# Kernel tuning notes

Hardware: AMD Instinct MI355X
Metric: run time of the kernel (lower is better)

## Reference

```python
import jax, jax.numpy as jnp
import numpy as np

N_NODES = 100000


def gcn_conv(x, W, b, src, dst, n_nodes):
    """PyG-style GCNConv: h = D^{-1/2} (A + I) D^{-1/2} (x @ W) + b.

    src/dst already include self-loops. Symmetric normalization with
    degrees computed on the destination index (in-degree incl. self-loop).
    """
    h = x @ W  # [N, out] - transform before propagate (cheap gather dim)
    deg = jax.ops.segment_sum(jnp.ones_like(dst, dtype=h.dtype), dst,
                              num_segments=n_nodes)  # [N]
    dinv = jnp.where(deg > 0, jax.lax.rsqrt(deg), 0.0)  # deg^{-1/2}, 0 for isolated
    norm = dinv[src] * dinv[dst]  # [E]
    msg = h[src] * norm[:, None]  # gather + normalize, [E, out]
    out = jax.ops.segment_sum(msg, dst, num_segments=n_nodes)  # scatter-sum
    return out + b


def setup_inputs() -> dict:
    key = jax.random.key(0)
    k1, k2, k3, k4 = jax.random.split(key, 4)
    in_dim, hidden, n_edges = 128, 32, 3200000
    x = jax.random.normal(k1, (N_NODES, in_dim), dtype=jnp.float32)
    edge_index = jax.random.randint(k2, (2, n_edges), 0, N_NODES, dtype=jnp.int64)
    W1 = jax.random.normal(k3, (in_dim, hidden), dtype=jnp.float32) / np.sqrt(in_dim)
    b1 = jnp.zeros((hidden,), dtype=jnp.float32)
    W2 = jax.random.normal(k4, (hidden, 1), dtype=jnp.float32) / np.sqrt(hidden)
    b2 = jnp.zeros((1,), dtype=jnp.float32)
    return {"x": x, "edge_index": edge_index, "W1": W1, "b1": b1,
            "W2": W2, "b2": b2}


def reference(x, edge_index, W1, b1, W2, b2):
    n = x.shape[0]
    loops = jnp.arange(n, dtype=edge_index.dtype)
    src = jnp.concatenate([edge_index[0], loops])  # add self-loops
    dst = jnp.concatenate([edge_index[1], loops])
    h = jax.nn.relu(gcn_conv(x, W1, b1, src, dst, n))
    out = jax.nn.sigmoid(gcn_conv(h, W2, b2, src, dst, n))
    return out.squeeze(-1)  # [N]
```

## Files before the change

kernel.cpp:

```cpp
#include <hip/hip_runtime.h>
#include <hip/hip_bf16.h>
#include <stdint.h>

#define IN_DIM 128
#define HID 32
#define CSHIFT 7
#define CNODES 128
#define CAP 4608
#define NPART 8
#define SUBCAP 672
#define TILE 4096
#define NBC_MAX 800

__device__ __forceinline__ float bf_lo(uint u) {
    uint t = u << 16; return *(float*)&t;
}
__device__ __forceinline__ float bf_hi(uint u) {
    uint t = u & 0xFFFF0000u; return *(float*)&t;
}

__global__ __launch_bounds__(256) void binB_kernel(const int* __restrict__ src,
                                                   const int* __restrict__ dst,
                                                   int* __restrict__ pcursor,
                                                   int* __restrict__ pbuf,
                                                   int e, int nbc) {
    __shared__ int pk[TILE];
    __shared__ short binsArr[TILE];
    __shared__ int hist[NBC_MAX];
    __shared__ int gbase[NBC_MAX];
    int part = blockIdx.x & (NPART - 1);
    int base = blockIdx.x * TILE;
    int cnt = min(TILE, e - base);
    if (cnt <= 0) return;
    for (int i = threadIdx.x; i < nbc; i += 256) hist[i] = 0;
    __syncthreads();
    for (int i = threadIdx.x; i < cnt; i += 256) {
        int s = __builtin_nontemporal_load(src + base + i);
        int d = __builtin_nontemporal_load(dst + base + i);
        int bin = d >> CSHIFT;
        pk[i] = s | ((d & (CNODES - 1)) << 17);
        binsArr[i] = (short)bin;
        atomicAdd(&hist[bin], 1);
    }
    __syncthreads();
    for (int i = threadIdx.x; i < nbc; i += 256) {
        int c = hist[i];
        gbase[i] = (c > 0) ? atomicAdd(&pcursor[part * nbc + i], c) : 0;
        hist[i] = 0;
    }
    __syncthreads();
    for (int i = threadIdx.x; i < cnt; i += 256) {
        int bin = binsArr[i];
        int slot = atomicAdd(&hist[bin], 1);
        int pos = gbase[bin] + slot;
        if (pos < SUBCAP)
            pbuf[(size_t)(part * nbc + bin) * SUBCAP + pos] = pk[i];
    }
}

__global__ __launch_bounds__(256) void sortmm_kernel(const int* __restrict__ pcursor,
                                                     const int* __restrict__ pbuf,
                                                     int* __restrict__ csr,
                                                     int* __restrict__ row_beg,
                                                     int* __restrict__ row_end,
                                                     float* __restrict__ dinv_g,
                                                     const float* __restrict__ x,
                                                     const float* __restrict__ W1,
                                                     __hip_bfloat16* __restrict__ h1s,
                                                     int n, int nbc) {
    int b = blockIdx.x;
    __shared__ int sbe[CAP];
    __shared__ int hist[CNODES];
    __shared__ int offs[CNODES];
    __shared__ int cur[CNODES];
    __shared__ int scnt[NPART + 1];
    int tid = threadIdx.x;
    if (tid == 0) {
        int run = 0;
        for (int p = 0; p < NPART; p++) {
            scnt[p] = run;
            run += min(pcursor[p * nbc + b], SUBCAP);
        }
        scnt[NPART] = run;
    }
    if (tid < CNODES) hist[tid] = 0;
    __syncthreads();
    for (int p = 0; p < NPART; p++) {
        int cnt = scnt[p + 1] - scnt[p];
        const int* seg = pbuf + (size_t)(p * nbc + b) * SUBCAP;
        int dstoff = scnt[p];
        for (int i = tid; i < cnt; i += 256) {
            int v = __builtin_nontemporal_load(seg + i);
            if (dstoff + i < CAP) {
                sbe[dstoff + i] = v;
                atomicAdd(&hist[v >> 17], 1);
            }
        }
    }
    __syncthreads();
    if (tid < 64) {
        int lane = tid;
        int b2 = lane * 2;
        int s0 = hist[b2], s1 = hist[b2 + 1];
        int lsum = s0 + s1;
        int pref = lsum;
#pragma unroll
        for (int m = 1; m < 64; m <<= 1) {
            int t = __shfl_up(pref, m);
            if (lane >= m) pref += t;
        }
        pref -= lsum;
        offs[b2] = pref;           cur[b2] = pref;
        offs[b2 + 1] = pref + s0;  cur[b2 + 1] = pref + s0;
    }
    __syncthreads();
    int total = min(scnt[NPART], CAP);
    int base = b * CAP;
    for (int i = tid; i < total; i += 256) {
        int p = sbe[i];
        int pos = atomicAdd(&cur[p >> 17], 1);
        csr[base + pos] = p & 0x1FFFF;
    }
    if (tid < CNODES) {
        int node = b * CNODES + tid;
        if (node < n) {
            int o = offs[tid], h = hist[tid];
            row_beg[node] = base + o;
            row_end[node] = base + o + h;
            dinv_g[node] = rsqrtf((float)h + 1.0f);
        }
    }
    __syncthreads();
    float* Ws = (float*)sbe;
    for (int i = tid; i < IN_DIM * HID; i += 256) Ws[i] = W1[i];
    __syncthreads();
    int node2 = b * CNODES + (tid >> 1);
    int khalf = tid & 1;
    if (node2 >= n) return;
    float dv = rsqrtf((float)hist[tid >> 1] + 1.0f);
    float acc[HID];
#pragma unroll
    for (int j = 0; j < HID; j++) acc[j] = 0.f;
    const float4* xr = (const float4*)(x + (size_t)node2 * IN_DIM + khalf * 64);
    int kbase = khalf * 64;
#pragma unroll 4
    for (int k4 = 0; k4 < 16; k4++) {
        float4 xv = xr[k4];
        int k = kbase + k4 * 4;
#pragma unroll
        for (int j = 0; j < HID; j++) {
            acc[j] += xv.x * Ws[(k + 0) * HID + j] + xv.y * Ws[(k + 1) * HID + j]
                    + xv.z * Ws[(k + 2) * HID + j] + xv.w * Ws[(k + 3) * HID + j];
        }
    }
#pragma unroll
    for (int j = 0; j < HID; j++) acc[j] += __shfl_xor(acc[j], 1);
    uint pkd[8];
    int abase = khalf * 16;
#pragma unroll
    for (int q = 0; q < 8; q++) {
        __hip_bfloat162 p2 = __float22bfloat162_rn(
            make_float2(acc[abase + 2 * q] * dv, acc[abase + 2 * q + 1] * dv));
        pkd[q] = *(uint*)&p2;
    }
    uint4* o = (uint4*)(h1s + (size_t)node2 * HID) + khalf * 2;
    o[0] = make_uint4(pkd[0], pkd[1], pkd[2], pkd[3]);
    o[1] = make_uint4(pkd[4], pkd[5], pkd[6], pkd[7]);
}

__global__ __launch_bounds__(256) void gather1_kernel(const int* __restrict__ row_beg,
                                                      const int* __restrict__ row_end,
                                                      const int* __restrict__ csr,
                                                      const float* __restrict__ dinv,
                                                      const __hip_bfloat16* __restrict__ h1s,
                                                      const float* __restrict__ b1,
                                                      const float* __restrict__ W2,
                                                      float* __restrict__ h2s, int n) {
    int wave = (blockIdx.x * 256 + threadIdx.x) >> 6;
    int gwaves = (gridDim.x * 256) >> 6;
    int lane = threadIdx.x & 63;
    int j2 = lane & 15;
    int quad = lane >> 4;
    const uint* h1u = (const uint*)h1s;
    float b1a = b1[2 * j2], b1b = b1[2 * j2 + 1];
    float w2a = W2[2 * j2], w2b = W2[2 * j2 + 1];
    for (int d = wave; d < n; d += gwaves) {
        int beg = row_beg[d], end = row_end[d];
        float a0 = 0.f, a1 = 0.f;
        int p = beg + quad;
        for (; p + 12 < end; p += 16) {
            int s0 = csr[p];
            int s1 = csr[p + 4];
            int s2 = csr[p + 8];
            int s3 = csr[p + 12];
            uint u0 = h1u[(size_t)s0 * 16 + j2];
            uint u1 = h1u[(size_t)s1 * 16 + j2];
            uint u2 = h1u[(size_t)s2 * 16 + j2];
            uint u3 = h1u[(size_t)s3 * 16 + j2];
            a0 += bf_lo(u0) + bf_lo(u1) + bf_lo(u2) + bf_lo(u3);
            a1 += bf_hi(u0) + bf_hi(u1) + bf_hi(u2) + bf_hi(u3);
        }
        for (; p < end; p += 4) {
            uint u = h1u[(size_t)csr[p] * 16 + j2];
            a0 += bf_lo(u);
            a1 += bf_hi(u);
        }
        a0 += __shfl_xor(a0, 16);  a0 += __shfl_xor(a0, 32);
        a1 += __shfl_xor(a1, 16);  a1 += __shfl_xor(a1, 32);
        float dd = dinv[d];
        uint su = h1u[(size_t)d * 16 + j2];
        float v0 = (a0 + bf_lo(su)) * dd + b1a;
        float v1 = (a1 + bf_hi(su)) * dd + b1b;
        v0 = fmaxf(v0, 0.f);
        v1 = fmaxf(v1, 0.f);
        float pv = v0 * w2a + v1 * w2b;
#pragma unroll
        for (int m = 1; m < 16; m <<= 1) pv += __shfl_xor(pv, m);
        if (lane == 0) h2s[d] = pv * dd;
    }
}

__global__ __launch_bounds__(256) void gather2_kernel(const int* __restrict__ row_beg,
                                                      const int* __restrict__ row_end,
                                                      const int* __restrict__ csr,
                                                      const float* __restrict__ dinv,
                                                      const float* __restrict__ h2s,
                                                      const float* __restrict__ b2,
                                                      float* __restrict__ out, int n) {
    int hw = (blockIdx.x * 256 + threadIdx.x) >> 5;
    int ghw = (gridDim.x * 256) >> 5;
    int l = threadIdx.x & 31;
    float bias = b2[0];
    for (int d = hw; d < n; d += ghw) {
        int beg = row_beg[d], end = row_end[d];
        float acc = 0.f;
        for (int p = beg + l; p < end; p += 32) {
            acc += h2s[csr[p]];
        }
#pragma unroll
        for (int m = 1; m < 32; m <<= 1) acc += __shfl_xor(acc, m, 32);
        if (l == 0) {
            float dd = dinv[d];
            float v = (acc + h2s[d]) * dd + bias;
            out[d] = 1.f / (1.f + expf(-v));
        }
    }
}

extern "C" void kernel_launch(void* const* d_in, const int* in_sizes, int n_in,
                              void* d_out, int out_size, void* d_ws, size_t ws_size,
                              hipStream_t stream) {
    const float* x  = (const float*)d_in[0];
    const int*   ei = (const int*)d_in[1];
    const float* W1 = (const float*)d_in[2];
    const float* b1 = (const float*)d_in[3];
    const float* W2 = (const float*)d_in[4];
    const float* b2 = (const float*)d_in[5];
    float* out = (float*)d_out;

    const int n = in_sizes[0] / IN_DIM;
    const int e = in_sizes[1] / 2;
    const int* src = ei;
    const int* dst = ei + e;
    const int nbc = (n + CNODES - 1) >> CSHIFT;

    int*   pbuf    = (int*)d_ws;
    int*   csr     = pbuf + (size_t)NPART * nbc * SUBCAP;
    __hip_bfloat16* h1s = (__hip_bfloat16*)(csr + (size_t)nbc * CAP);
    float* dinv    = (float*)(h1s + (size_t)n * HID);
    float* h2s     = dinv + n;
    int*   row_beg = (int*)(h2s + n);
    int*   row_end = row_beg + n;
    int*   pcursor = row_end + n;

    const int B = 256;
    int gBin = (e + TILE - 1) / TILE;
    int gP = 2048;
    int m  = NPART * nbc;

    hipMemsetAsync(pcursor, 0, (size_t)m * sizeof(int), stream);
    binB_kernel<<<gBin, B, 0, stream>>>(src, dst, pcursor, pbuf, e, nbc);
    sortmm_kernel<<<nbc, B, 0, stream>>>(pcursor, pbuf, csr, row_beg, row_end, dinv,
                                         x, W1, h1s, n, nbc);
    gather1_kernel<<<gP, B, 0, stream>>>(row_beg, row_end, csr, dinv, h1s, b1, W2, h2s, n);
    gather2_kernel<<<gP, B, 0, stream>>>(row_beg, row_end, csr, dinv, h2s, b2, out, n);
}
```

Measured before the change: 252.4 us.

## Drop binning LDS staging, parallelize partition prefix, and pad W1 halves

```diff
diff --git a/kernel.cpp b/kernel.cpp
--- a/kernel.cpp
+++ b/kernel.cpp
@@ -11,6 +11,7 @@
 #define SUBCAP 672
 #define TILE 4096
 #define NBC_MAX 800
+#define WS_ODD 2052
 
 __device__ __forceinline__ float bf_lo(uint u) {
     uint t = u << 16; return *(float*)&t;
@@ -24,8 +25,6 @@
                                                    int* __restrict__ pcursor,
                                                    int* __restrict__ pbuf,
                                                    int e, int nbc) {
-    __shared__ int pk[TILE];
-    __shared__ short binsArr[TILE];
     __shared__ int hist[NBC_MAX];
     __shared__ int gbase[NBC_MAX];
     int part = blockIdx.x & (NPART - 1);
@@ -35,12 +34,8 @@
     for (int i = threadIdx.x; i < nbc; i += 256) hist[i] = 0;
     __syncthreads();
     for (int i = threadIdx.x; i < cnt; i += 256) {
-        int s = __builtin_nontemporal_load(src + base + i);
-        int d = __builtin_nontemporal_load(dst + base + i);
-        int bin = d >> CSHIFT;
-        pk[i] = s | ((d & (CNODES - 1)) << 17);
-        binsArr[i] = (short)bin;
-        atomicAdd(&hist[bin], 1);
+        int d = dst[base + i];
+        atomicAdd(&hist[d >> CSHIFT], 1);
     }
     __syncthreads();
     for (int i = threadIdx.x; i < nbc; i += 256) {
@@ -50,11 +45,13 @@
     }
     __syncthreads();
     for (int i = threadIdx.x; i < cnt; i += 256) {
-        int bin = binsArr[i];
+        int s = src[base + i];
+        int d = dst[base + i];
+        int bin = d >> CSHIFT;
         int slot = atomicAdd(&hist[bin], 1);
         int pos = gbase[bin] + slot;
         if (pos < SUBCAP)
-            pbuf[(size_t)(part * nbc + bin) * SUBCAP + pos] = pk[i];
+            pbuf[(size_t)(part * nbc + bin) * SUBCAP + pos] = s | ((d & (CNODES - 1)) << 17);
     }
 }
 
@@ -75,13 +72,17 @@
     __shared__ int cur[CNODES];
     __shared__ int scnt[NPART + 1];
     int tid = threadIdx.x;
-    if (tid == 0) {
-        int run = 0;
-        for (int p = 0; p < NPART; p++) {
-            scnt[p] = run;
-            run += min(pcursor[p * nbc + b], SUBCAP);
-        }
-        scnt[NPART] = run;
+    if (tid < 64) {
+        int lane = tid;
+        int c = (lane < NPART) ? min(pcursor[lane * nbc + b], SUBCAP) : 0;
+        int pref = c;
+#pragma unroll
+        for (int m = 1; m < 8; m <<= 1) {
+            int t = __shfl_up(pref, m);
+            if (lane >= m) pref += t;
+        }
+        if (lane < NPART) scnt[lane + 1] = pref;
+        if (lane == 0) scnt[0] = 0;
     }
     if (tid < CNODES) hist[tid] = 0;
     __syncthreads();
@@ -132,7 +133,8 @@
     }
     __syncthreads();
     float* Ws = (float*)sbe;
-    for (int i = tid; i < IN_DIM * HID; i += 256) Ws[i] = W1[i];
+    for (int i = tid; i < IN_DIM * HID; i += 256)
+        Ws[i + ((i >= 2048) ? 4 : 0)] = W1[i];
     __syncthreads();
     int node2 = b * CNODES + (tid >> 1);
     int khalf = tid & 1;
@@ -142,15 +144,15 @@
 #pragma unroll
     for (int j = 0; j < HID; j++) acc[j] = 0.f;
     const float4* xr = (const float4*)(x + (size_t)node2 * IN_DIM + khalf * 64);
-    int kbase = khalf * 64;
+    const float* Wh = Ws + (khalf ? WS_ODD : 0);
 #pragma unroll 4
     for (int k4 = 0; k4 < 16; k4++) {
         float4 xv = xr[k4];
-        int k = kbase + k4 * 4;
+        int k = k4 * 4;
 #pragma unroll
         for (int j = 0; j < HID; j++) {
-            acc[j] += xv.x * Ws[(k + 0) * HID + j] + xv.y * Ws[(k + 1) * HID + j]
-                    + xv.z * Ws[(k + 2) * HID + j] + xv.w * Ws[(k + 3) * HID + j];
+            acc[j] += xv.x * Wh[(k + 0) * HID + j] + xv.y * Wh[(k + 1) * HID + j]
+                    + xv.z * Wh[(k + 2) * HID + j] + xv.w * Wh[(k + 3) * HID + j];
         }
     }
 #pragma unroll
```

Result: faster. 242.3 us (-4.0%).
